# Performance work log

Measured on AMD Instinct MI355X. Metric: run time of the kernel, lower is better.

Reference implementation:

```python
import jax, jax.numpy as jnp
import numpy as np

B, S, D, H = 2, 2048, 1024, 16
HD = D // H
SCALE = HD ** -0.5

def setup_inputs() -> dict:
    key = jax.random.key(0)
    ks = jax.random.split(key, 5)
    x = jax.random.normal(ks[0], (B, S, D), dtype=jnp.float32)
    Wqkv = jax.random.normal(ks[1], (D, 3 * D), dtype=jnp.float32) * (D ** -0.5)
    bqkv = jnp.zeros((3 * D,), dtype=jnp.float32)
    Wproj = jax.random.normal(ks[2], (D, D), dtype=jnp.float32) * (D ** -0.5)
    bproj = jnp.zeros((D,), dtype=jnp.float32)
    return {"x": x, "Wqkv": Wqkv, "bqkv": bqkv, "Wproj": Wproj, "bproj": bproj}

def reference(x, Wqkv, bqkv, Wproj, bproj):
    b, s, _ = x.shape
    qkv = x @ Wqkv + bqkv                       # [B,S,3D]
    qkv = qkv.reshape(b, s, 3, H, HD)
    q, k, v = [jnp.transpose(qkv[:, :, i], (0, 2, 1, 3)) for i in range(3)]  # [B,H,S,HD]
    attn = jnp.einsum('bhqd,bhkd->bhqk', q, k) * SCALE   # [B,H,S,S]
    attn = jax.nn.softmax(attn, axis=-1)
    out = jnp.einsum('bhqk,bhkd->bhqd', attn, v)         # [B,H,S,HD]
    out = jnp.transpose(out, (0, 2, 1, 3)).reshape(b, s, D)
    return out @ Wproj + bproj
```

## Files before the change

kernel.cpp:

```cpp
#include <hip/hip_runtime.h>
#include <hip/hip_bf16.h>

#define BB 2
#define SS 2048
#define DD 1024
#define HH 16
#define HDD 64
#define MM (BB*SS)
#define NQKV (3*DD)
#define SCALE 0.125f
#define QPRESCALE 0.18033688f

typedef __bf16 bf16_t;
typedef bf16_t bf16x4 __attribute__((ext_vector_type(4)));
typedef bf16_t bf16x8 __attribute__((ext_vector_type(8)));
typedef float f32x4 __attribute__((ext_vector_type(4)));
typedef float f32x16 __attribute__((ext_vector_type(16)));

__device__ __forceinline__ void gl_lds16(const bf16_t* g, bf16_t* l) {
    __builtin_amdgcn_global_load_lds(
        (const __attribute__((address_space(1))) unsigned int*)(uintptr_t)g,
        (__attribute__((address_space(3))) unsigned int*)(uintptr_t)l,
        16, 0, 0);
}

__device__ __forceinline__ f32x4 MF(bf16x8 a, bf16x8 b, f32x4 c) {
    return __builtin_amdgcn_mfma_f32_16x16x32_bf16(a, b, c, 0, 0, 0);
}

__global__ __launch_bounds__(256) void prep(
    const float* __restrict__ x, const float* __restrict__ Wqkv,
    const float* __restrict__ Wproj, bf16_t* __restrict__ xb,
    bf16_t* __restrict__ wqkvt, bf16_t* __restrict__ wprojt)
{
    const int bx = blockIdx.x;
    if (bx < 2048) {
        int i = (bx * 256 + threadIdx.x) * 8;
        float4 a = *(const float4*)(x + i);
        float4 b = *(const float4*)(x + i + 4);
        bf16x8 v;
        v[0]=(bf16_t)a.x; v[1]=(bf16_t)a.y; v[2]=(bf16_t)a.z; v[3]=(bf16_t)a.w;
        v[4]=(bf16_t)b.x; v[5]=(bf16_t)b.y; v[6]=(bf16_t)b.z; v[7]=(bf16_t)b.w;
        *reinterpret_cast<bf16x8*>(xb + i) = v;
        return;
    }
    __shared__ float tile[32][33];
    const float* src; bf16_t* dst; int C, bxl, byl;
    if (bx < 5120) {
        int t = bx - 2048;
        byl = t / 96; bxl = t - byl * 96;
        src = Wqkv;  dst = wqkvt;  C = NQKV;
    } else {
        int t = bx - 5120;
        byl = t >> 5; bxl = t & 31;
        src = Wproj; dst = wprojt; C = DD;
    }
    const int R = DD;
    const int tx = threadIdx.x & 31, ty = threadIdx.x >> 5;
    const int r0 = byl * 32, c0 = bxl * 32;
    #pragma unroll
    for (int i = 0; i < 32; i += 8)
        tile[ty + i][tx] = src[(size_t)(r0 + ty + i) * C + c0 + tx];
    __syncthreads();
    #pragma unroll
    for (int i = 0; i < 32; i += 8)
        dst[(size_t)(c0 + ty + i) * R + r0 + tx] = (bf16_t)tile[tx][ty + i];
}

__global__ __launch_bounds__(512, 2) void gemm_qkv(
    const bf16_t* __restrict__ A, const bf16_t* __restrict__ Bt,
    const float* __restrict__ bias,
    bf16_t* __restrict__ qw, bf16_t* __restrict__ kw, bf16_t* __restrict__ vtw)
{
    constexpr int K  = DD;
    constexpr int BM = 256, BN = 192, BK = 64;
    constexpr int NT = K / BK;

    __shared__ __align__(16) bf16_t smem[2 * BM * BK + 2 * BN * BK];
    bf16_t* const As0 = smem;
    bf16_t* const As1 = smem + BM * BK;
    bf16_t* const Bs0 = smem + 2 * BM * BK;
    bf16_t* const Bs1 = Bs0 + BN * BK;

    const int tid  = threadIdx.x;
    const int w    = tid >> 6;
    const int lane = tid & 63;
    const int lr   = lane & 15;
    const int quad = lane >> 4;
    const int wm   = w >> 2;
    const int wn   = w & 3;
    const int m0   = blockIdx.y * BM;
    const int n0   = blockIdx.x * BN;

    const int sx   = lr & 7;
    const int ecc0 = ((quad)     ^ sx) * 8;
    const int ecc1 = ((quad + 4) ^ sx) * 8;
    const int aOff = (wm * 128 + lr) * BK;
    const int bOff = (wn * 48  + lr) * BK;

    f32x4 acc[2][4][3];
    #pragma unroll
    for (int mh = 0; mh < 2; mh++)
        #pragma unroll
        for (int mi = 0; mi < 4; mi++)
            #pragma unroll
            for (int ni = 0; ni < 3; ni++)
                acc[mh][mi][ni] = (f32x4){0.f, 0.f, 0.f, 0.f};

    auto stageA = [&](int kt, bf16_t* dst) {
        #pragma unroll
        for (int r = 0; r < 4; ++r) {
            const int c   = r * 512 + tid;
            const int row = c >> 3;
            const int cg  = (c & 7) ^ (row & 7);
            gl_lds16(A + (size_t)(m0 + row) * K + kt * BK + cg * 8, dst + c * 8);
        }
    };
    auto stageB = [&](int kt, bf16_t* dst) {
        #pragma unroll
        for (int r = 0; r < 3; ++r) {
            const int c   = r * 512 + tid;
            const int row = c >> 3;
            const int cg  = (c & 7) ^ (row & 7);
            gl_lds16(Bt + (size_t)(n0 + row) * K + kt * BK + cg * 8, dst + c * 8);
        }
    };

    stageA(0, As0);
    stageB(0, Bs0);
    asm volatile("s_waitcnt vmcnt(0)" ::: "memory");
    __builtin_amdgcn_s_barrier();

    auto tile = [&](int t, const bf16_t* Ac, const bf16_t* Bc,
                    bf16_t* An, bf16_t* Bn) {
        const bool more = (t + 1) < NT;
        bf16x8 af[4], bk0[3], bk1[3];

        #pragma unroll
        for (int mi = 0; mi < 4; mi++)
            af[mi] = *(const bf16x8*)(Ac + aOff + mi * 16 * BK + ecc0);
        #pragma unroll
        for (int ni = 0; ni < 3; ni++)
            bk0[ni] = *(const bf16x8*)(Bc + bOff + ni * 16 * BK + ecc0);
        if (more) stageA(t + 1, An);
        __builtin_amdgcn_s_barrier();
        __builtin_amdgcn_sched_barrier(0);
        __builtin_amdgcn_s_setprio(1);
        #pragma unroll
        for (int mi = 0; mi < 4; mi++)
            #pragma unroll
            for (int ni = 0; ni < 3; ni++)
                acc[0][mi][ni] = MF(af[mi], bk0[ni], acc[0][mi][ni]);
        __builtin_amdgcn_s_setprio(0);
        __builtin_amdgcn_sched_barrier(0);
        __builtin_amdgcn_s_barrier();

        #pragma unroll
        for (int mi = 0; mi < 4; mi++)
            af[mi] = *(const bf16x8*)(Ac + aOff + mi * 16 * BK + ecc1);
        #pragma unroll
        for (int ni = 0; ni < 3; ni++)
            bk1[ni] = *(const bf16x8*)(Bc + bOff + ni * 16 * BK + ecc1);
        if (more) stageB(t + 1, Bn);
        __builtin_amdgcn_s_barrier();
        __builtin_amdgcn_sched_barrier(0);
        __builtin_amdgcn_s_setprio(1);
        #pragma unroll
        for (int mi = 0; mi < 4; mi++)
            #pragma unroll
            for (int ni = 0; ni < 3; ni++)
                acc[0][mi][ni] = MF(af[mi], bk1[ni], acc[0][mi][ni]);
        __builtin_amdgcn_s_setprio(0);
        __builtin_amdgcn_sched_barrier(0);
        __builtin_amdgcn_s_barrier();

        #pragma unroll
        for (int mi = 0; mi < 4; mi++)
            af[mi] = *(const bf16x8*)(Ac + aOff + (64 + mi * 16) * BK + ecc1);
        __builtin_amdgcn_s_barrier();
        __builtin_amdgcn_sched_barrier(0);
        __builtin_amdgcn_s_setprio(1);
        #pragma unroll
        for (int mi = 0; mi < 4; mi++)
            #pragma unroll
            for (int ni = 0; ni < 3; ni++)
                acc[1][mi][ni] = MF(af[mi], bk1[ni], acc[1][mi][ni]);
        __builtin_amdgcn_s_setprio(0);
        __builtin_amdgcn_sched_barrier(0);
        __builtin_amdgcn_s_barrier();

        #pragma unroll
        for (int mi = 0; mi < 4; mi++)
            af[mi] = *(const bf16x8*)(Ac + aOff + (64 + mi * 16) * BK + ecc0);
        __builtin_amdgcn_s_barrier();
        __builtin_amdgcn_sched_barrier(0);
        __builtin_amdgcn_s_setprio(1);
        #pragma unroll
        for (int mi = 0; mi < 4; mi++)
            #pragma unroll
            for (int ni = 0; ni < 3; ni++)
                acc[1][mi][ni] = MF(af[mi], bk0[ni], acc[1][mi][ni]);
        __builtin_amdgcn_s_setprio(0);
        __builtin_amdgcn_sched_barrier(0);
        if (more) asm volatile("s_waitcnt vmcnt(0)" ::: "memory");
        __builtin_amdgcn_s_barrier();
    };

    #pragma unroll 1
    for (int tt = 0; tt < NT; tt += 2) {
        tile(tt,     As0, Bs0, As1, Bs1);
        tile(tt + 1, As1, Bs1, As0, Bs0);
    }

    #pragma unroll
    for (int mh = 0; mh < 2; mh++) {
        #pragma unroll
        for (int mi = 0; mi < 4; mi++) {
            #pragma unroll
            for (int ni = 0; ni < 3; ni++) {
                const int col = n0 + wn * 48 + ni * 16 + lr;
                const float bcol = bias[col];
                const int which = col >> 10;
                const int d = col & 1023;
                const int h = d >> 6, hd = d & 63;
                #pragma unroll
                for (int reg = 0; reg < 4; reg++) {
                    const int row = m0 + wm * 128 + mh * 64 + mi * 16 + quad * 4 + reg;
                    const float val = acc[mh][mi][ni][reg] + bcol;
                    const int b = row >> 11, s = row & 2047;
                    const size_t bh = (size_t)(b * HH + h);
                    if (which == 0)      qw[(bh * SS + s) * HDD + hd] = (bf16_t)(val * QPRESCALE);
                    else if (which == 1) kw[(bh * SS + s) * HDD + hd] = (bf16_t)val;
                    else                 vtw[(bh * HDD + hd) * SS + s] = (bf16_t)val;
                }
            }
        }
    }
}

__global__ __launch_bounds__(256) void gemm_bt64(
    const bf16_t* __restrict__ A, const bf16_t* __restrict__ Bt,
    const float* __restrict__ bias, float* __restrict__ outf, int N, int K)
{
    __shared__ __align__(16) bf16_t As[2][64 * 32];
    __shared__ __align__(16) bf16_t Bs[2][128 * 32];

    const int tid  = threadIdx.x;
    const int w    = tid >> 6;
    const int lane = tid & 63;
    const int lr   = lane & 15;
    const int quad = lane >> 4;
    const int m0   = blockIdx.y * 64;
    const int n0   = blockIdx.x * 128;
    const int wm   = w >> 1;
    const int wn   = w & 1;

    f32x4 acc[2][4];
    #pragma unroll
    for (int i = 0; i < 2; i++)
        #pragma unroll
        for (int j = 0; j < 4; j++) acc[i][j] = (f32x4){0.f, 0.f, 0.f, 0.f};

    const int stgRow = lane >> 2;
    const int stgCol = (lane & 3) * 8;
    const bf16_t* aPtr = A  + (size_t)(m0 + w * 16 + stgRow) * K + stgCol;
    const bf16_t* bPtr = Bt + (size_t)(n0 + w * 32 + stgRow) * K + stgCol;
    const size_t rowSkip = (size_t)16 * K;

    for (int ks = 0; ks < K; ks += 64) {
        __syncthreads();
        #pragma unroll
        for (int s = 0; s < 2; s++) {
            const int ko = ks + s * 32;
            gl_lds16(aPtr + ko,           &As[s][w * 512]);
            gl_lds16(bPtr + ko,           &Bs[s][w * 1024]);
            gl_lds16(bPtr + rowSkip + ko, &Bs[s][w * 1024 + 512]);
        }
        __syncthreads();

        #pragma unroll
        for (int s = 0; s < 2; s++) {
            bf16x8 af[2], bf[4];
            #pragma unroll
            for (int mi = 0; mi < 2; mi++)
                af[mi] = *reinterpret_cast<const bf16x8*>(&As[s][(wm * 32 + mi * 16 + lr) * 32 + quad * 8]);
            #pragma unroll
            for (int ni = 0; ni < 4; ni++)
                bf[ni] = *reinterpret_cast<const bf16x8*>(&Bs[s][(wn * 64 + ni * 16 + lr) * 32 + quad * 8]);
            #pragma unroll
            for (int mi = 0; mi < 2; mi++)
                #pragma unroll
                for (int ni = 0; ni < 4; ni++)
                    acc[mi][ni] = __builtin_amdgcn_mfma_f32_16x16x32_bf16(af[mi], bf[ni], acc[mi][ni], 0, 0, 0);
        }
    }

    #pragma unroll
    for (int mi = 0; mi < 2; mi++)
        #pragma unroll
        for (int ni = 0; ni < 4; ni++)
            #pragma unroll
            for (int reg = 0; reg < 4; reg++) {
                int row = m0 + wm * 32 + mi * 16 + quad * 4 + reg;
                int col = n0 + wn * 64 + ni * 16 + lr;
                outf[(size_t)row * N + col] = acc[mi][ni][reg] + bias[col];
            }
}

__global__ __launch_bounds__(512, 4) void attn_kernel(
    const bf16_t* __restrict__ qws, const bf16_t* __restrict__ kws,
    const bf16_t* __restrict__ vtws, bf16_t* __restrict__ ob)
{
    __shared__ __align__(16) bf16_t smem[34048];
    bf16_t* Ks = smem;
    bf16_t* Vs = smem + 16640;

    const int tid  = threadIdx.x;
    const int w    = tid >> 6;
    const int g    = w >> 2;
    const int wg   = w & 3;
    const int lane = tid & 63;
    const int ln31 = lane & 31;
    const int ln5  = lane >> 5;

    const int qb = blockIdx.x;
    const int bh = blockIdx.y;
    const int b  = bh >> 4;
    const int h  = bh & 15;

    const bf16_t* Qh  = qws  + (size_t)bh * SS * HDD;
    const bf16_t* Kh  = kws  + (size_t)bh * SS * HDD;
    const bf16_t* Vth = vtws + (size_t)bh * HDD * SS;

    const int q0w    = qb * 128 + wg * 32;
    const int kvbase = g * 1024;

    bf16x8 aq[4];
    #pragma unroll
    for (int f = 0; f < 4; f++)
        aq[f] = *(const bf16x8*)(Qh + (size_t)(q0w + ln31) * HDD + f * 16 + ln5 * 8);

    const int gtid = tid & 255;
    const int sc = gtid & 7;
    const int sr = gtid >> 3;

    {
        const int ko = g * 520;
        const int vo = g * 4352;
        bf16x8 k0 = *(const bf16x8*)(Kh  + (size_t)(kvbase + sr     ) * HDD + sc * 8);
        bf16x8 k1 = *(const bf16x8*)(Kh  + (size_t)(kvbase + sr + 32) * HDD + sc * 8);
        bf16x8 v0 = *(const bf16x8*)(Vth + (size_t)(sr     ) * SS + kvbase + sc * 8);
        bf16x8 v1 = *(const bf16x8*)(Vth + (size_t)(sr + 32) * SS + kvbase + sc * 8);
        *reinterpret_cast<bf16x8*>(&Ks[(ko + sc * 65 + sr     ) * 8]) = k0;
        *reinterpret_cast<bf16x8*>(&Ks[(ko + sc * 65 + sr + 32) * 8]) = k1;
        bf16_t* vd0 = &Vs[vo + (sr     ) * 68 + sc * 8];
        bf16_t* vd1 = &Vs[vo + (sr + 32) * 68 + sc * 8];
        *reinterpret_cast<bf16x4*>(vd0)     = __builtin_shufflevector(v0, v0, 0,1,2,3);
        *reinterpret_cast<bf16x4*>(vd0 + 4) = __builtin_shufflevector(v0, v0, 4,5,6,7);
        *reinterpret_cast<bf16x4*>(vd1)     = __builtin_shufflevector(v1, v1, 0,1,2,3);
        *reinterpret_cast<bf16x4*>(vd1 + 4) = __builtin_shufflevector(v1, v1, 4,5,6,7);
    }
    __syncthreads();

    float l = 0.f;
    f32x16 o[2];
    #pragma unroll
    for (int nh = 0; nh < 2; nh++)
        #pragma unroll
        for (int r = 0; r < 16; r++) o[nh][r] = 0.f;

    int buf = 0;
    for (int it = 0; it < 16; ++it) {
        const int ko = buf * 1040 + g * 520;
        const int vo = buf * 8704 + g * 4352;

        f32x16 sfr[2];
        #pragma unroll
        for (int ni = 0; ni < 2; ni++) {
            #pragma unroll
            for (int r = 0; r < 16; r++) sfr[ni][r] = 0.f;
            #pragma unroll
            for (int f = 0; f < 4; f++) {
                bf16x8 kb = *reinterpret_cast<const bf16x8*>(
                    &Ks[(ko + (2 * f + ln5) * 65 + ni * 32 + ln31) * 8]);
                sfr[ni] = __builtin_amdgcn_mfma_f32_32x32x16_bf16(kb, aq[f], sfr[ni], 0, 0, 0);
            }
        }

        bf16x8 nk0, nk1, nv0, nv1;
        const bool more = (it + 1 < 16);
        if (more) {
            const int kvn = kvbase + (it + 1) * 64;
            nk0 = *(const bf16x8*)(Kh  + (size_t)(kvn + sr     ) * HDD + sc * 8);
            nk1 = *(const bf16x8*)(Kh  + (size_t)(kvn + sr + 32) * HDD + sc * 8);
            nv0 = *(const bf16x8*)(Vth + (size_t)(sr     ) * SS + kvn + sc * 8);
            nv1 = *(const bf16x8*)(Vth + (size_t)(sr + 32) * SS + kvn + sc * 8);
        }

        float p[2][16];
        #pragma unroll
        for (int ni = 0; ni < 2; ni++)
            #pragma unroll
            for (int r = 0; r < 16; r++) {
                p[ni][r] = __builtin_amdgcn_exp2f(sfr[ni][r]);
                l += p[ni][r];
            }

        bf16x8 ap[4];
        #pragma unroll
        for (int c16 = 0; c16 < 4; c16++)
            #pragma unroll
            for (int j = 0; j < 8; j++)
                ap[c16][j] = (bf16_t)p[c16 >> 1][(c16 & 1) * 8 + j];

        #pragma unroll
        for (int nh = 0; nh < 2; nh++) {
            const bf16_t* vrow = &Vs[vo + (nh * 32 + ln31) * 68];
            #pragma unroll
            for (int c16 = 0; c16 < 4; c16++) {
                bf16x4 lo = *(const bf16x4*)(vrow + c16 * 16 + 4 * ln5);
                bf16x4 hi = *(const bf16x4*)(vrow + c16 * 16 + 8 + 4 * ln5);
                bf16x8 vb = __builtin_shufflevector(lo, hi, 0, 1, 2, 3, 4, 5, 6, 7);
                o[nh] = __builtin_amdgcn_mfma_f32_32x32x16_bf16(ap[c16], vb, o[nh], 0, 0, 0);
            }
        }

        if (more) {
            const int ko1 = (buf ^ 1) * 1040 + g * 520;
            const int vo1 = (buf ^ 1) * 8704 + g * 4352;
            *reinterpret_cast<bf16x8*>(&Ks[(ko1 + sc * 65 + sr     ) * 8]) = nk0;
            *reinterpret_cast<bf16x8*>(&Ks[(ko1 + sc * 65 + sr + 32) * 8]) = nk1;
            bf16_t* vd0 = &Vs[vo1 + (sr     ) * 68 + sc * 8];
            bf16_t* vd1 = &Vs[vo1 + (sr + 32) * 68 + sc * 8];
            *reinterpret_cast<bf16x4*>(vd0)     = __builtin_shufflevector(nv0, nv0, 0,1,2,3);
            *reinterpret_cast<bf16x4*>(vd0 + 4) = __builtin_shufflevector(nv0, nv0, 4,5,6,7);
            *reinterpret_cast<bf16x4*>(vd1)     = __builtin_shufflevector(nv1, nv1, 0,1,2,3);
            *reinterpret_cast<bf16x4*>(vd1 + 4) = __builtin_shufflevector(nv1, nv1, 4,5,6,7);
        }
        __syncthreads();
        buf ^= 1;
    }

    l += __shfl_xor(l, 32, 64);

    __syncthreads();
    float* Of = (float*)smem;
    float* Lf = (float*)(smem + 16384);
    if (ln5 == 0) Lf[g * 128 + wg * 32 + ln31] = l;
    if (g == 1) {
        #pragma unroll
        for (int nh = 0; nh < 2; nh++)
            #pragma unroll
            for (int r = 0; r < 16; r++) {
                const int q = (r & 3) + 8 * (r >> 2) + 4 * ln5;
                Of[(wg * 32 + q) * 64 + nh * 32 + ln31] = o[nh][r];
            }
    }
    __syncthreads();
    if (g == 0) {
        float inv[16];
        #pragma unroll
        for (int r = 0; r < 16; r++) {
            const int q = (r & 3) + 8 * (r >> 2) + 4 * ln5;
            inv[r] = 1.f / (Lf[wg * 32 + q] + Lf[128 + wg * 32 + q]);
        }
        #pragma unroll
        for (int nh = 0; nh < 2; nh++)
            #pragma unroll
            for (int r = 0; r < 16; r++) {
                const int q  = (r & 3) + 8 * (r >> 2) + 4 * ln5;
                const int hd = nh * 32 + ln31;
                float val = (o[nh][r] + Of[(wg * 32 + q) * 64 + hd]) * inv[r];
                ob[((size_t)b * SS + q0w + q) * DD + h * HDD + hd] = (bf16_t)val;
            }
    }
}

extern "C" void kernel_launch(void* const* d_in, const int* in_sizes, int n_in,
                              void* d_out, int out_size, void* d_ws, size_t ws_size,
                              hipStream_t stream) {
    const float* x     = (const float*)d_in[0];
    const float* Wqkv  = (const float*)d_in[1];
    const float* bqkv  = (const float*)d_in[2];
    const float* Wproj = (const float*)d_in[3];
    const float* bproj = (const float*)d_in[4];
    float* out = (float*)d_out;

    const size_t NEL = (size_t)MM * DD;
    bf16_t* qws    = (bf16_t*)d_ws;
    bf16_t* kws    = qws  + NEL;
    bf16_t* vtws   = kws  + NEL;
    bf16_t* xb     = vtws + NEL;
    bf16_t* ows    = xb;
    bf16_t* wqkvt  = xb + NEL;
    bf16_t* wprojt = wqkvt + (size_t)NQKV * DD;

    prep<<<6144, 256, 0, stream>>>(x, Wqkv, Wproj, xb, wqkvt, wprojt);

    gemm_qkv<<<dim3(NQKV / 192, MM / 256), 512, 0, stream>>>(
        xb, wqkvt, bqkv, qws, kws, vtws);

    attn_kernel<<<dim3(SS / 128, BB * HH), 512, 0, stream>>>(qws, kws, vtws, ows);

    gemm_bt64<<<dim3(DD / 128, MM / 64), 256, 0, stream>>>(
        ows, wprojt, bproj, out, DD, DD);
}
```

Baseline: 192.5 us.

## Restructure QKV GEMM tile into two k-halves and stage V transpose through LDS

The inner tile loop drops from four barrier-separated MFMA phases to two. Each phase now loads all eight A fragments and one set of B fragments, and both next-tile stages are issued up front. The epilogue now packs the V-transpose outputs into LDS and writes them back as 16-byte coalesced stores along the sequence dimension, replacing scattered 2-byte strided stores. This reduces barrier count and uncoalesced global writes, but raises register pressure from the larger fragment arrays and reuses shared memory after the final barrier.

```diff
diff --git a/kernel.cpp b/kernel.cpp
--- a/kernel.cpp
+++ b/kernel.cpp
@@ -134,72 +134,48 @@
     auto tile = [&](int t, const bf16_t* Ac, const bf16_t* Bc,
                     bf16_t* An, bf16_t* Bn) {
         const bool more = (t + 1) < NT;
-        bf16x8 af[4], bk0[3], bk1[3];
-
-        #pragma unroll
-        for (int mi = 0; mi < 4; mi++)
-            af[mi] = *(const bf16x8*)(Ac + aOff + mi * 16 * BK + ecc0);
+        bf16x8 af[8], bk[3];
+
+        #pragma unroll
+        for (int mi = 0; mi < 4; mi++) {
+            af[mi]     = *(const bf16x8*)(Ac + aOff + mi * 16 * BK + ecc0);
+            af[4 + mi] = *(const bf16x8*)(Ac + aOff + (64 + mi * 16) * BK + ecc0);
+        }
         #pragma unroll
         for (int ni = 0; ni < 3; ni++)
-            bk0[ni] = *(const bf16x8*)(Bc + bOff + ni * 16 * BK + ecc0);
-        if (more) stageA(t + 1, An);
+            bk[ni] = *(const bf16x8*)(Bc + bOff + ni * 16 * BK + ecc0);
+        if (more) { stageA(t + 1, An); stageB(t + 1, Bn); }
         __builtin_amdgcn_s_barrier();
         __builtin_amdgcn_sched_barrier(0);
         __builtin_amdgcn_s_setprio(1);
         #pragma unroll
-        for (int mi = 0; mi < 4; mi++)
-            #pragma unroll
-            for (int ni = 0; ni < 3; ni++)
-                acc[0][mi][ni] = MF(af[mi], bk0[ni], acc[0][mi][ni]);
+        for (int mh = 0; mh < 2; mh++)
+            #pragma unroll
+            for (int mi = 0; mi < 4; mi++)
+                #pragma unroll
+                for (int ni = 0; ni < 3; ni++)
+                    acc[mh][mi][ni] = MF(af[mh * 4 + mi], bk[ni], acc[mh][mi][ni]);
         __builtin_amdgcn_s_setprio(0);
         __builtin_amdgcn_sched_barrier(0);
-        __builtin_amdgcn_s_barrier();
-
-        #pragma unroll
-        for (int mi = 0; mi < 4; mi++)
-            af[mi] = *(const bf16x8*)(Ac + aOff + mi * 16 * BK + ecc1);
+
+        #pragma unroll
+        for (int mi = 0; mi < 4; mi++) {
+            af[mi]     = *(const bf16x8*)(Ac + aOff + mi * 16 * BK + ecc1);
+            af[4 + mi] = *(const bf16x8*)(Ac + aOff + (64 + mi * 16) * BK + ecc1);
+        }
         #pragma unroll
         for (int ni = 0; ni < 3; ni++)
-            bk1[ni] = *(const bf16x8*)(Bc + bOff + ni * 16 * BK + ecc1);
-        if (more) stageB(t + 1, Bn);
+            bk[ni] = *(const bf16x8*)(Bc + bOff + ni * 16 * BK + ecc1);
         __builtin_amdgcn_s_barrier();
         __builtin_amdgcn_sched_barrier(0);
         __builtin_amdgcn_s_setprio(1);
         #pragma unroll
-        for (int mi = 0; mi < 4; mi++)
-            #pragma unroll
-            for (int ni = 0; ni < 3; ni++)
-                acc[0][mi][ni] = MF(af[mi], bk1[ni], acc[0][mi][ni]);
-        __builtin_amdgcn_s_setprio(0);
-        __builtin_amdgcn_sched_barrier(0);
-        __builtin_amdgcn_s_barrier();
-
-        #pragma unroll
-        for (int mi = 0; mi < 4; mi++)
-            af[mi] = *(const bf16x8*)(Ac + aOff + (64 + mi * 16) * BK + ecc1);
-        __builtin_amdgcn_s_barrier();
-        __builtin_amdgcn_sched_barrier(0);
-        __builtin_amdgcn_s_setprio(1);
-        #pragma unroll
-        for (int mi = 0; mi < 4; mi++)
-            #pragma unroll
-            for (int ni = 0; ni < 3; ni++)
-                acc[1][mi][ni] = MF(af[mi], bk1[ni], acc[1][mi][ni]);
-        __builtin_amdgcn_s_setprio(0);
-        __builtin_amdgcn_sched_barrier(0);
-        __builtin_amdgcn_s_barrier();
-
-        #pragma unroll
-        for (int mi = 0; mi < 4; mi++)
-            af[mi] = *(const bf16x8*)(Ac + aOff + (64 + mi * 16) * BK + ecc0);
-        __builtin_amdgcn_s_barrier();
-        __builtin_amdgcn_sched_barrier(0);
-        __builtin_amdgcn_s_setprio(1);
-        #pragma unroll
-        for (int mi = 0; mi < 4; mi++)
-            #pragma unroll
-            for (int ni = 0; ni < 3; ni++)
-                acc[1][mi][ni] = MF(af[mi], bk0[ni], acc[1][mi][ni]);
+        for (int mh = 0; mh < 2; mh++)
+            #pragma unroll
+            for (int mi = 0; mi < 4; mi++)
+                #pragma unroll
+                for (int ni = 0; ni < 3; ni++)
+                    acc[mh][mi][ni] = MF(af[mh * 4 + mi], bk[ni], acc[mh][mi][ni]);
         __builtin_amdgcn_s_setprio(0);
         __builtin_amdgcn_sched_barrier(0);
         if (more) asm volatile("s_waitcnt vmcnt(0)" ::: "memory");
@@ -212,28 +188,65 @@
         tile(tt + 1, As1, Bs1, As0, Bs0);
     }
 
+    __builtin_amdgcn_s_barrier();
+
+    const int colBase = n0 + wn * 48;
+    const int vbase   = (n0 < 2048) ? 2048 : n0;
     #pragma unroll
     for (int mh = 0; mh < 2; mh++) {
         #pragma unroll
-        for (int mi = 0; mi < 4; mi++) {
-            #pragma unroll
-            for (int ni = 0; ni < 3; ni++) {
-                const int col = n0 + wn * 48 + ni * 16 + lr;
-                const float bcol = bias[col];
-                const int which = col >> 10;
-                const int d = col & 1023;
-                const int h = d >> 6, hd = d & 63;
-                #pragma unroll
-                for (int reg = 0; reg < 4; reg++) {
-                    const int row = m0 + wm * 128 + mh * 64 + mi * 16 + quad * 4 + reg;
-                    const float val = acc[mh][mi][ni][reg] + bcol;
-                    const int b = row >> 11, s = row & 2047;
-                    const size_t bh = (size_t)(b * HH + h);
-                    if (which == 0)      qw[(bh * SS + s) * HDD + hd] = (bf16_t)(val * QPRESCALE);
-                    else if (which == 1) kw[(bh * SS + s) * HDD + hd] = (bf16_t)val;
-                    else                 vtw[(bh * HDD + hd) * SS + s] = (bf16_t)val;
+        for (int ni = 0; ni < 3; ni++) {
+            const int col = colBase + ni * 16 + lr;
+            const float bcol = bias[col];
+            const int which = col >> 10;
+            const int d = col & 1023;
+            const int h = d >> 6, hd = d & 63;
+            #pragma unroll
+            for (int mi = 0; mi < 4; mi++) {
+                const int rl0 = wm * 128 + mh * 64 + mi * 16 + quad * 4;
+                if (which == 0) {
+                    #pragma unroll
+                    for (int reg = 0; reg < 4; reg++) {
+                        const int row = m0 + rl0 + reg;
+                        const int b = row >> 11, s = row & 2047;
+                        qw[(((size_t)(b * HH + h)) * SS + s) * HDD + hd] =
+                            (bf16_t)((acc[mh][mi][ni][reg] + bcol) * QPRESCALE);
+                    }
+                } else if (which == 1) {
+                    #pragma unroll
+                    for (int reg = 0; reg < 4; reg++) {
+                        const int row = m0 + rl0 + reg;
+                        const int b = row >> 11, s = row & 2047;
+                        kw[(((size_t)(b * HH + h)) * SS + s) * HDD + hd] =
+                            (bf16_t)(acc[mh][mi][ni][reg] + bcol);
+                    }
+                } else {
+                    bf16x4 pk;
+                    #pragma unroll
+                    for (int reg = 0; reg < 4; reg++)
+                        pk[reg] = (bf16_t)(acc[mh][mi][ni][reg] + bcol);
+                    const int lc = col - vbase;
+                    *reinterpret_cast<bf16x4*>(&smem[lc * 264 + rl0]) = pk;
                 }
             }
+        }
+    }
+    const int nv = n0 + BN - 2048;
+    if (nv > 0) {
+        __builtin_amdgcn_s_barrier();
+        const int nvc = nv < BN ? nv : BN;
+        const int lcb = tid >> 5;
+        const int rl  = (tid & 31) * 8;
+        const int b   = m0 >> 11;
+        const int s   = (m0 & 2047) + rl;
+        for (int j = 0; j < nvc / 16; j++) {
+            const int lc = j * 16 + lcb;
+            bf16x8 vv = *reinterpret_cast<const bf16x8*>(&smem[lc * 264 + rl]);
+            const int col = vbase + lc;
+            const int d = col & 1023;
+            const int h = d >> 6, hd = d & 63;
+            *reinterpret_cast<bf16x8*>(
+                vtw + (((size_t)(b * HH + h)) * HDD + hd) * SS + s) = vv;
         }
     }
 }
```

New measurement: 179.8 us. 6.6% less time.
